# Kernel tuning notes

Hardware: AMD Instinct MI355X
Metric: run time of the kernel (lower is better)

Reference implementation:

```python
import jax, jax.numpy as jnp
import numpy as np

L, N, D, B_, T = 4, 4, 2048, 2, 2048  # num_blocks, expansion_rate, dim, batch, seq


def setup_inputs() -> dict:
    key = jax.random.key(0)
    ks = jax.random.split(key, 12)
    f = lambda k, sh, s=0.02: s * jax.random.normal(k, sh, jnp.float32)
    x = jax.random.normal(ks[0], (B_, T, D), jnp.float32)
    # structural torch inits + small noise so grads/kernels are exercised
    eyecols = jnp.stack([jnp.eye(N, dtype=jnp.float32)[:, [i % N]] for i in range(L)])  # [L,N,1]
    A_m = eyecols + f(ks[1], (L, N, 1), 0.05)
    A_r = jnp.broadcast_to(jnp.eye(N, dtype=jnp.float32), (L, N, N)) + f(ks[2], (L, N, N), 0.05)
    Bp = jnp.ones((L, 1, N), jnp.float32) + f(ks[3], (L, 1, N), 0.05)
    W_m = f(ks[4], (L, D, 1))
    W_r = f(ks[5], (L, D, N))
    W_b = f(ks[6], (L, D, N))
    s_a = 0.01 * jnp.ones((L, 1, 1), jnp.float32)
    s_b = 0.01 * jnp.ones((L, 1, 1), jnp.float32)
    dyn_gamma = jnp.ones((L, D), jnp.float32) + f(ks[7], (L, D), 0.05)   # LayerNorm(bias=False)
    norm_gamma = jnp.ones((L, D), jnp.float32) + f(ks[8], (L, D), 0.05)  # per-block norm weight
    norm_beta = f(ks[9], (L, D))                                          # per-block norm bias
    Wblk = f(ks[10], (L, D, D), 1.0) / np.sqrt(D)                         # block = Linear(D, D)
    bblk = f(ks[11], (L, D))
    return dict(x=x, A_m=A_m, A_r=A_r, Bp=Bp, W_m=W_m, W_r=W_r, W_b=W_b,
                s_a=s_a, s_b=s_b, dyn_gamma=dyn_gamma, norm_gamma=norm_gamma,
                norm_beta=norm_beta, Wblk=Wblk, bblk=bblk)


def _ln(x, gamma, beta=None, eps=1e-5):
    mu = jnp.mean(x, axis=-1, keepdims=True)
    var = jnp.mean(jnp.square(x - mu), axis=-1, keepdims=True)
    y = (x - mu) * jax.lax.rsqrt(var + eps) * gamma
    return y if beta is None else y + beta


def reference(x, A_m, A_r, Bp, W_m, W_r, W_b, s_a, s_b,
              dyn_gamma, norm_gamma, norm_beta, Wblk, bblk):
    # hyper branch (n > 0), dynamic=True, pre_norm=True
    H = jnp.repeat(x[:, :, None, :], N, axis=2)  # [B,T,N,D]
    for i in range(L):
        # ---- width connections ----
        Hn = _ln(H, dyn_gamma[i])                                              # dynamic LN, no bias
        Am = A_m[i] + s_a[i] * jnp.tanh(jnp.einsum('btnd,do->btno', Hn, W_m[i]))  # [B,T,N,1]
        Ar = A_r[i] + s_a[i] * jnp.tanh(jnp.einsum('btnd,dm->btnm', Hn, W_r[i]))  # [B,T,N,N]
        WC = jnp.concatenate([Am, Ar], axis=-1)                                # [B,T,N,1+N]
        Ht = jnp.einsum('btnd,btnm->btdm', H, WC)                              # H^T @ WC
        h = Ht[..., 0]                                                         # [B,T,D]
        H = jnp.swapaxes(Ht[..., 1:], -2, -1)                                  # [B,T,N,D]
        # ---- pre-norm + block ----
        h = _ln(h, norm_gamma[i], norm_beta[i])
        h = jnp.einsum('btd,de->bte', h, Wblk[i]) + bblk[i]
        # ---- depth connections ----
        hn = _ln(h, dyn_gamma[i])
        Bv = Bp[i][0] + s_b[i] * jnp.tanh(jnp.einsum('btd,dn->btn', hn, W_b[i]))  # [B,T,N]
        H = H + h[:, :, None, :] * Bv[..., None]
    return H.sum(axis=2)  # [B,T,D]
```

## Files before the change

### kernel.cpp

```cpp
#include <hip/hip_runtime.h>
#include <hip/hip_bf16.h>


#define DD 2048
#define NN 4
#define LL 4
#define NTOK 4096
#define EPSF 1e-5f
#define STS 80

typedef __attribute__((ext_vector_type(8))) short bf16x8;
typedef __attribute__((ext_vector_type(4))) float f32x4;
typedef __attribute__((ext_vector_type(2))) float f32x2;

__device__ __forceinline__ float bf2f(short u) {
  union { unsigned int i; float f; } v;
  v.i = ((unsigned int)(unsigned short)u) << 16;
  return v.f;
}
__device__ __forceinline__ short f2bf(float f) {
  __hip_bfloat16 h = __float2bfloat16(f);
  short s;
  __builtin_memcpy(&s, &h, 2);
  return s;
}
__device__ __forceinline__ float wred(float v) {
#pragma unroll
  for (int off = 32; off > 0; off >>= 1) v += __shfl_xor(v, off, 64);
  return v;
}
__device__ __forceinline__ void ld16(const void* g, void* l) {
  __builtin_amdgcn_global_load_lds(
      (const __attribute__((address_space(1))) void*)g,
      (__attribute__((address_space(3))) void*)l, 16, 0, 0);
}
__host__ __device__ constexpr int pofs(int k, int l) {
  return k == 0 ? 20 + l * 5
       : k == 1 ? 40 + (l - 1) * 5
       : k == 2 ? 55 + (l - 2) * 5
                : 65;
}

__global__ __launch_bounds__(256) void prep_pack(
    const float* __restrict__ W_m, const float* __restrict__ W_r,
    const float* __restrict__ W_b, const float* __restrict__ dyn_gamma,
    const float* __restrict__ norm_gamma, const float* __restrict__ norm_beta,
    short* __restrict__ gwm, short* __restrict__ gwr, short* __restrict__ gwb,
    float* __restrict__ rb) {
  const int i = blockIdx.x * 256 + threadIdx.x;
  const float g = dyn_gamma[i];
  gwm[i] = f2bf(g * W_m[i]);
  f32x4 r = *(const f32x4*)(W_r + (size_t)i * 4);
  f32x4 b = *(const f32x4*)(W_b + (size_t)i * 4);
  short ro[4], bo[4];
#pragma unroll
  for (int k = 0; k < 4; k++) { ro[k] = f2bf(g * r[k]); bo[k] = f2bf(g * b[k]); }
  *(unsigned long long*)(gwr + (size_t)i * 4) = *(unsigned long long*)ro;
  *(unsigned long long*)(gwb + (size_t)i * 4) = *(unsigned long long*)bo;
  rb[i] = norm_beta[i] / norm_gamma[i];
}

__global__ __launch_bounds__(64) void prep_sums(
    const float* __restrict__ W_m, const float* __restrict__ W_r,
    const float* __restrict__ W_b, const float* __restrict__ dyn_gamma,
    float* __restrict__ S0w, float* __restrict__ T0d) {
  const int l = blockIdx.x;
  const int lane = threadIdx.x;
  float s[5] = {0, 0, 0, 0, 0}, t[4] = {0, 0, 0, 0};
  for (int d = lane; d < DD; d += 64) {
    const float g = dyn_gamma[l * DD + d];
    s[0] += g * W_m[l * DD + d];
    f32x4 r = *(const f32x4*)(W_r + ((size_t)l * DD + d) * 4);
    f32x4 b = *(const f32x4*)(W_b + ((size_t)l * DD + d) * 4);
#pragma unroll
    for (int m = 0; m < 4; m++) { s[1 + m] += g * r[m]; t[m] += g * b[m]; }
  }
#pragma unroll
  for (int m = 0; m < 5; m++) s[m] = wred(s[m]);
#pragma unroll
  for (int n = 0; n < 4; n++) t[n] = wred(t[n]);
  if (lane == 0) {
#pragma unroll
    for (int m = 0; m < 5; m++) S0w[l * 5 + m] = s[m];
#pragma unroll
    for (int n = 0; n < 4; n++) T0d[l * 4 + n] = t[n];
  }
}

__global__ __launch_bounds__(256) void transpose_wblk(
    const float* __restrict__ W, const float* __restrict__ norm_gamma,
    short* __restrict__ Wt) {
  __shared__ float tile[64][65];
  const int blk = blockIdx.z;
  const int c0 = blockIdx.x * 64;
  const int r0 = blockIdx.y * 64;
  const float* Ws = W + (size_t)blk * DD * DD;
  short* Wd = Wt + (size_t)blk * DD * DD;
  const int tx = threadIdx.x & 63, ty = threadIdx.x >> 6;
#pragma unroll
  for (int r = 0; r < 16; r++) {
    const int row = ty + r * 4;
    tile[row][tx] = Ws[(size_t)(r0 + row) * DD + c0 + tx];
  }
  const float gsc = norm_gamma[blk * DD + r0 + tx];
  __syncthreads();
#pragma unroll
  for (int r = 0; r < 16; r++) {
    const int row = ty + r * 4;
    Wd[(size_t)(c0 + row) * DD + r0 + tx] = f2bf(tile[tx][row] * gsc);
  }
}

__global__ __launch_bounds__(256) void row_sums(
    const short* __restrict__ Wt, const float* __restrict__ rb,
    const float* __restrict__ bblk, float* __restrict__ E0,
    float* __restrict__ E1) {
  const int l = blockIdx.y;
  const int e = blockIdx.x * 4 + (threadIdx.x >> 6);
  const int lane = threadIdx.x & 63;
  const short* row = Wt + ((size_t)l * DD + e) * DD;
  const float* rbl = rb + l * DD;
  float s1 = 0.f, s0 = 0.f;
#pragma unroll
  for (int it = 0; it < 4; it++) {
    const int d0 = lane * 8 + it * 512;
    bf16x8 w = *(const bf16x8*)(row + d0);
    f32x4 r0 = *(const f32x4*)(rbl + d0), r1 = *(const f32x4*)(rbl + d0 + 4);
#pragma unroll
    for (int q = 0; q < 8; q++) {
      const float wq = bf2f(w[q]);
      s1 += wq;
      s0 += wq * ((q < 4) ? r0[q] : r1[q - 4]);
    }
  }
  s1 = wred(s1); s0 = wred(s0);
  if (lane == 0) {
    E1[l * DD + e] = s1;
    E0[l * DD + e] = s0 + bblk[l * DD + e];
  }
}

__global__ __launch_bounds__(256) void width0_kernel(
    const float* __restrict__ x, short* __restrict__ b0,
    short* __restrict__ hout, f32x2* __restrict__ tst, float* __restrict__ Cc,
    float* __restrict__ ST, const float* __restrict__ A_m,
    const float* __restrict__ A_r, const short* __restrict__ gwm,
    const short* __restrict__ gwr, const float* __restrict__ s_a,
    const float* __restrict__ S0w) {
  const int wave = threadIdx.x >> 6;
  const int lane = threadIdx.x & 63;
  const int tok = blockIdx.x * 4 + wave;
  const float* xr = x + (size_t)tok * DD;
  short* b0t = b0 + (size_t)tok * DD;

  bf16x8 xb[4];
#pragma unroll
  for (int j = 0; j < 4; j++) {
    const int d0 = lane * 8 + j * 512;
    f32x4 a = *(const f32x4*)(xr + d0);
    f32x4 b = *(const f32x4*)(xr + d0 + 4);
    bf16x8 p;
#pragma unroll
    for (int q = 0; q < 4; q++) { p[q] = f2bf(a[q]); p[4 + q] = f2bf(b[q]); }
    xb[j] = p;
    *(bf16x8*)(b0t + d0) = p;
  }

  float o = 0.f, qq = 0.f, P0[4][5];
#pragma unroll
  for (int l = 0; l < 4; l++)
#pragma unroll
    for (int m = 0; m < 5; m++) P0[l][m] = 0.f;

#pragma unroll
  for (int j = 0; j < 4; j++) {
    const int d0 = lane * 8 + j * 512;
    bf16x8 wmv[4], wrv[4][4];
#pragma unroll
    for (int l = 0; l < 4; l++) {
      wmv[l] = *(const bf16x8*)(gwm + l * DD + d0);
#pragma unroll
      for (int p = 0; p < 4; p++)
        wrv[l][p] = *(const bf16x8*)(gwr + ((size_t)l * DD + d0 + 2 * p) * 4);
    }
#pragma unroll
    for (int q = 0; q < 8; q++) {
      const float hv = bf2f(xb[j][q]);
      o += hv; qq += hv * hv;
#pragma unroll
      for (int l = 0; l < 4; l++) {
        P0[l][0] += hv * bf2f(wmv[l][q]);
#pragma unroll
        for (int m = 0; m < 4; m++)
          P0[l][1 + m] += hv * bf2f(wrv[l][q >> 1][(q & 1) * 4 + m]);
      }
    }
  }
  o = wred(o); qq = wred(qq);
#pragma unroll
  for (int l = 0; l < 4; l++)
#pragma unroll
    for (int m = 0; m < 5; m++) P0[l][m] = wred(P0[l][m]);

  const float sa = s_a[0];
  const float mu = o * (1.f / DD);
  const float inv = rsqrtf(qq * (1.f / DD) - mu * mu + EPSF);
  const float t0 = tanhf(inv * (P0[0][0] - mu * S0w[0]));
  float tm[4];
#pragma unroll
  for (int m = 0; m < 4; m++)
    tm[m] = tanhf(inv * (P0[0][1 + m] - mu * S0w[1 + m]));
  float amSum = 0.f, arCol[4] = {0, 0, 0, 0};
#pragma unroll
  for (int n = 0; n < 4; n++) {
    amSum += A_m[n] + sa * t0;
#pragma unroll
    for (int m = 0; m < 4; m++) arCol[m] += A_r[n * 4 + m] + sa * tm[m];
  }

  if (lane == 0) {
    const float sh = amSum * o;
    const float sh2 = amSum * amSum * qq;
    const float mu2 = sh * (1.f / DD);
    const float inv2 = rsqrtf(sh2 * (1.f / DD) - mu2 * mu2 + EPSF);
    f32x2 t; t[0] = inv2; t[1] = mu2 * inv2;
    tst[tok] = t;
    float* STt = ST + (size_t)tok * STS;
    STt[0] = o;
    STt[4] = qq;
#pragma unroll
    for (int l = 0; l < 4; l++)
#pragma unroll
      for (int m = 0; m < 5; m++) STt[pofs(0, l) + m] = P0[l][m];
    float* Ct = Cc + (size_t)tok * 16;
#pragma unroll
    for (int n = 0; n < 4; n++) Ct[n * 4] = arCol[n];
  }

  short* hw = hout + (size_t)tok * DD;
#pragma unroll
  for (int j = 0; j < 4; j++) {
    const int d0 = lane * 8 + j * 512;
    bf16x8 ho;
#pragma unroll
    for (int q = 0; q < 8; q++) ho[q] = f2bf(amSum * bf2f(xb[j][q]));
    *(bf16x8*)(hw + d0) = ho;
  }
}

__global__ __launch_bounds__(512) void gemm_kernel(
    const short* __restrict__ A, const short* __restrict__ Bt,
    const f32x2* __restrict__ tst, const float* __restrict__ E0,
    const float* __restrict__ E1, short* __restrict__ C) {
  __shared__ short lA[2][128 * 64];
  __shared__ short lB[2][128 * 64];
  const int tid = threadIdx.x;
  const int lane = tid & 63;
  const int wave = tid >> 6;
  const int bid = blockIdx.x;
  const int wg = (bid & 7) * 64 + (bid >> 3);
  const int m0 = (wg & 31) * 128, n0 = (wg >> 5) * 128;
  const int wm = wave >> 2;
  const int wn = wave & 3;

  f32x4 acc[4][2] = {};

#define STAGE(buf, kt)                                                        \
  {                                                                           \
    const int k0 = (kt) * 64;                                                 \
    _Pragma("unroll") for (int c = 0; c < 2; c++) {                           \
      const int idx = c * 512 + tid;                                          \
      const int row = idx >> 3;                                               \
      const int colsw = (((idx & 7) ^ (row & 7)) * 8);                        \
      ld16(A + (size_t)(m0 + row) * DD + k0 + colsw,                          \
           (char*)&lA[buf][0] + idx * 16);                                    \
      ld16(Bt + (size_t)(n0 + row) * DD + k0 + colsw,                         \
           (char*)&lB[buf][0] + idx * 16);                                    \
    }                                                                         \
  }

  STAGE(0, 0);
  __syncthreads();

  for (int kt = 0; kt < 32; ++kt) {
    const int cur = kt & 1;
    if (kt < 31) STAGE(cur ^ 1, kt + 1);
    const char* bufA = (const char*)&lA[cur][0];
    const char* bufB = (const char*)&lB[cur][0];
#pragma unroll
    for (int kk = 0; kk < 2; ++kk) {
      const int gsw = (kk * 64 + (lane >> 4) * 16) ^ ((lane & 7) << 4);
      bf16x8 af[4], bfr[2];
#pragma unroll
      for (int m = 0; m < 4; m++) {
        const int r = wm * 64 + m * 16 + (lane & 15);
        af[m] = *(const bf16x8*)(bufA + r * 128 + gsw);
      }
#pragma unroll
      for (int n = 0; n < 2; n++) {
        const int r = wn * 32 + n * 16 + (lane & 15);
        bfr[n] = *(const bf16x8*)(bufB + r * 128 + gsw);
      }
#pragma unroll
      for (int m = 0; m < 4; m++)
#pragma unroll
        for (int n = 0; n < 2; n++)
          acc[m][n] = __builtin_amdgcn_mfma_f32_16x16x32_bf16(
              af[m], bfr[n], acc[m][n], 0, 0, 0);
    }
    __syncthreads();
  }
#undef STAGE

  float e0c[2], e1c[2];
  int cols[2];
#pragma unroll
  for (int n = 0; n < 2; n++) {
    cols[n] = n0 + wn * 32 + n * 16 + (lane & 15);
    e0c[n] = E0[cols[n]];
    e1c[n] = E1[cols[n]];
  }
#pragma unroll
  for (int m = 0; m < 4; m++) {
    const int rbase = m0 + wm * 64 + m * 16 + ((lane >> 4) << 2);
#pragma unroll
    for (int j = 0; j < 4; j++) {
      const int row = rbase + j;
      const f32x2 iv = tst[row];
#pragma unroll
      for (int n = 0; n < 2; n++)
        C[(size_t)row * DD + cols[n]] =
            f2bf(iv[0] * acc[m][n][j] - iv[1] * e1c[n] + e0c[n]);
    }
  }
}

template <int I>
__global__ __launch_bounds__(256) void fused_dw(
    const short* __restrict__ h2s, const short* __restrict__ b0,
    short* __restrict__ hout, f32x2* __restrict__ tst, float* __restrict__ Cc,
    float* __restrict__ ST, const float* __restrict__ Bp,
    const float* __restrict__ s_b, const float* __restrict__ A_m,
    const float* __restrict__ A_r, const float* __restrict__ s_a,
    const float* __restrict__ S0w, const float* __restrict__ T0d,
    const short* __restrict__ gwm, const short* __restrict__ gwr,
    const short* __restrict__ gwb) {
  constexpr int NB = I + 1;
  constexpr int NP = 3 - I;
  const int wave = threadIdx.x >> 6;
  const int lane = threadIdx.x & 63;
  const int tok = blockIdx.x * 4 + wave;

  const short* vt = h2s + ((size_t)I * NTOK + tok) * DD;
  const short* bases[I + 1];
  bases[0] = b0 + (size_t)tok * DD;
#pragma unroll
  for (int k = 1; k <= I; k++)
    bases[k] = h2s + ((size_t)(k - 1) * NTOK + tok) * DD;

  bf16x8 h2r[4];
#pragma unroll
  for (int j = 0; j < 4; j++)
    h2r[j] = *(const bf16x8*)(vt + lane * 8 + j * 512);

  float o = 0.f;
  float Gr[I + 2] = {};
  float Tb[4] = {0, 0, 0, 0};
  float Pn[NP][5];
#pragma unroll
  for (int li = 0; li < NP; li++)
#pragma unroll
    for (int m = 0; m < 5; m++) Pn[li][m] = 0.f;

#pragma unroll
  for (int j = 0; j < 4; j++) {
    const int d0 = lane * 8 + j * 512;
    bf16x8 bsv[I + 1];
#pragma unroll
    for (int k = 0; k <= I; k++) bsv[k] = *(const bf16x8*)(bases[k] + d0);
    bf16x8 wbv[4];
#pragma unroll
    for (int p = 0; p < 4; p++)
      wbv[p] = *(const bf16x8*)(gwb + ((size_t)I * DD + d0 + 2 * p) * 4);
    bf16x8 wmv[NP], wrv[NP][4];
#pragma unroll
    for (int li = 0; li < NP; li++) {
      const int l = NB + li;
      wmv[li] = *(const bf16x8*)(gwm + l * DD + d0);
#pragma unroll
      for (int p = 0; p < 4; p++)
        wrv[li][p] = *(const bf16x8*)(gwr + ((size_t)l * DD + d0 + 2 * p) * 4);
    }
#pragma unroll
    for (int q = 0; q < 8; q++) {
      const float hv = bf2f(h2r[j][q]);
      o += hv;
      Gr[I + 1] += hv * hv;
#pragma unroll
      for (int k = 0; k <= I; k++) Gr[k] += hv * bf2f(bsv[k][q]);
#pragma unroll
      for (int n = 0; n < 4; n++)
        Tb[n] += hv * bf2f(wbv[q >> 1][(q & 1) * 4 + n]);
#pragma unroll
      for (int li = 0; li < NP; li++) {
        Pn[li][0] += hv * bf2f(wmv[li][q]);
#pragma unroll
        for (int m = 0; m < 4; m++)
          Pn[li][1 + m] += hv * bf2f(wrv[li][q >> 1][(q & 1) * 4 + m]);
      }
    }
  }
  o = wred(o);
#pragma unroll
  for (int k = 0; k <= I + 1; k++) Gr[k] = wred(Gr[k]);
#pragma unroll
  for (int n = 0; n < 4; n++) Tb[n] = wred(Tb[n]);
#pragma unroll
  for (int li = 0; li < NP; li++)
#pragma unroll
    for (int m = 0; m < 5; m++) Pn[li][m] = wred(Pn[li][m]);

  float* STt = ST + (size_t)tok * STS;
  float* Ct = Cc + (size_t)tok * 16;
  float ofull[I + 2], Gf[I + 2][I + 2], Pf[I + 2][5], Cp[4][I + 2];
#pragma unroll
  for (int k = 0; k <= I; k++) ofull[k] = STt[k];
  ofull[I + 1] = o;
#pragma unroll
  for (int k = 0; k <= I; k++)
#pragma unroll
    for (int j2 = 0; j2 <= I; j2++) Gf[k][j2] = STt[4 + k * 4 + j2];
#pragma unroll
  for (int k = 0; k <= I; k++) { Gf[k][I + 1] = Gr[k]; Gf[I + 1][k] = Gr[k]; }
  Gf[I + 1][I + 1] = Gr[I + 1];
#pragma unroll
  for (int k = 0; k <= I; k++)
#pragma unroll
    for (int m = 0; m < 5; m++) Pf[k][m] = STt[pofs(k, NB) + m];
#pragma unroll
  for (int m = 0; m < 5; m++) Pf[I + 1][m] = Pn[0][m];
#pragma unroll
  for (int n = 0; n < 4; n++)
#pragma unroll
    for (int k = 0; k <= I; k++) Cp[n][k] = Ct[n * 4 + k];

  {
    const float mu2 = o * (1.f / DD);
    const float inv2 = rsqrtf(Gr[I + 1] * (1.f / DD) - mu2 * mu2 + EPSF);
    const float sb = s_b[I];
#pragma unroll
    for (int n = 0; n < 4; n++)
      Cp[n][I + 1] = Bp[I * 4 + n] +
                     sb * tanhf(inv2 * (Tb[n] - mu2 * T0d[I * 4 + n]));
  }

  const float sa = s_a[NB];
  float Am[4], Ar[4][4];
#pragma unroll
  for (int n = 0; n < 4; n++) {
    float sH = 0.f, sH2 = 0.f;
#pragma unroll
    for (int k = 0; k <= I + 1; k++) {
      sH += Cp[n][k] * ofull[k];
#pragma unroll
      for (int j2 = 0; j2 <= I + 1; j2++)
        sH2 += Cp[n][k] * Cp[n][j2] * Gf[k][j2];
    }
    const float mu = sH * (1.f / DD);
    const float inv = rsqrtf(sH2 * (1.f / DD) - mu * mu + EPSF);
    float S1[5];
#pragma unroll
    for (int m = 0; m < 5; m++) {
      S1[m] = 0.f;
#pragma unroll
      for (int k = 0; k <= I + 1; k++) S1[m] += Cp[n][k] * Pf[k][m];
    }
    Am[n] = A_m[NB * 4 + n] +
            sa * tanhf(inv * (S1[0] - mu * S0w[NB * 5 + 0]));
#pragma unroll
    for (int m = 0; m < 4; m++)
      Ar[n][m] = A_r[NB * 16 + n * 4 + m] +
                 sa * tanhf(inv * (S1[1 + m] - mu * S0w[NB * 5 + 1 + m]));
  }

  float Cn[4][I + 2], hc[I + 2];
#pragma unroll
  for (int k = 0; k <= I + 1; k++) {
    hc[k] = 0.f;
#pragma unroll
    for (int n = 0; n < 4; n++) hc[k] += Am[n] * Cp[n][k];
  }
#pragma unroll
  for (int mr = 0; mr < 4; mr++)
#pragma unroll
    for (int k = 0; k <= I + 1; k++) {
      float acc = 0.f;
#pragma unroll
      for (int n = 0; n < 4; n++) acc += Ar[n][mr] * Cp[n][k];
      Cn[mr][k] = acc;
    }

  if (lane == 0) {
    float sh = 0.f, sh2 = 0.f;
#pragma unroll
    for (int k = 0; k <= I + 1; k++) {
      sh += hc[k] * ofull[k];
#pragma unroll
      for (int j2 = 0; j2 <= I + 1; j2++) sh2 += hc[k] * hc[j2] * Gf[k][j2];
    }
    const float mu = sh * (1.f / DD);
    const float inv = rsqrtf(sh2 * (1.f / DD) - mu * mu + EPSF);
    f32x2 t; t[0] = inv; t[1] = mu * inv;
    tst[tok] = t;
    STt[I + 1] = o;
#pragma unroll
    for (int k = 0; k <= I + 1; k++) {
      STt[4 + (I + 1) * 4 + k] = Gf[I + 1][k];
      STt[4 + k * 4 + (I + 1)] = Gf[k][I + 1];
    }
#pragma unroll
    for (int li = 1; li < NP; li++)
#pragma unroll
      for (int m = 0; m < 5; m++) STt[pofs(I + 1, NB + li) + m] = Pn[li][m];
#pragma unroll
    for (int n = 0; n < 4; n++)
#pragma unroll
      for (int k = 0; k <= I + 1; k++) Ct[n * 4 + k] = Cn[n][k];
  }

  short* hw = hout + (size_t)tok * DD;
#pragma unroll
  for (int j = 0; j < 4; j++) {
    const int d0 = lane * 8 + j * 512;
    bf16x8 bsv[I + 1];
#pragma unroll
    for (int k = 0; k <= I; k++) bsv[k] = *(const bf16x8*)(bases[k] + d0);
    bf16x8 ho;
#pragma unroll
    for (int q = 0; q < 8; q++) {
      float a = hc[I + 1] * bf2f(h2r[j][q]);
#pragma unroll
      for (int k = 0; k <= I; k++) a += hc[k] * bf2f(bsv[k][q]);
      ho[q] = f2bf(a);
    }
    *(bf16x8*)(hw + d0) = ho;
  }
}

__global__ __launch_bounds__(256) void depth_last(
    const short* __restrict__ h2s, const short* __restrict__ b0,
    float* __restrict__ out, const float* __restrict__ Cc,
    const float* __restrict__ Bp, const float* __restrict__ s_b,
    const float* __restrict__ T0d, const short* __restrict__ gwb) {
  const int wave = threadIdx.x >> 6;
  const int lane = threadIdx.x & 63;
  const int tok = blockIdx.x * 4 + wave;
  const short* vt = h2s + ((size_t)3 * NTOK + tok) * DD;

  bf16x8 h2r[4];
  float s1 = 0.f, s2 = 0.f, Tb[4] = {0, 0, 0, 0};
#pragma unroll
  for (int j = 0; j < 4; j++) {
    const int d0 = lane * 8 + j * 512;
    h2r[j] = *(const bf16x8*)(vt + d0);
    bf16x8 wbv[4];
#pragma unroll
    for (int p = 0; p < 4; p++)
      wbv[p] = *(const bf16x8*)(gwb + ((size_t)3 * DD + d0 + 2 * p) * 4);
#pragma unroll
    for (int q = 0; q < 8; q++) {
      const float hv = bf2f(h2r[j][q]);
      s1 += hv; s2 += hv * hv;
#pragma unroll
      for (int n = 0; n < 4; n++)
        Tb[n] += hv * bf2f(wbv[q >> 1][(q & 1) * 4 + n]);
    }
  }
  s1 = wred(s1); s2 = wred(s2);
#pragma unroll
  for (int n = 0; n < 4; n++) Tb[n] = wred(Tb[n]);

  const float mu = s1 * (1.f / DD);
  const float inv = rsqrtf(s2 * (1.f / DD) - mu * mu + EPSF);
  const float sb = s_b[3];
  float bsum = 0.f;
#pragma unroll
  for (int n = 0; n < 4; n++)
    bsum += Bp[12 + n] + sb * tanhf(inv * (Tb[n] - mu * T0d[12 + n]));

  const float* Ct = Cc + (size_t)tok * 16;
  float e[4];
#pragma unroll
  for (int k = 0; k < 4; k++) {
    e[k] = 0.f;
#pragma unroll
    for (int n = 0; n < 4; n++) e[k] += Ct[n * 4 + k];
  }

  const short* bases[4];
  bases[0] = b0 + (size_t)tok * DD;
#pragma unroll
  for (int k = 1; k < 4; k++)
    bases[k] = h2s + ((size_t)(k - 1) * NTOK + tok) * DD;

  float* orow = out + (size_t)tok * DD;
#pragma unroll
  for (int j = 0; j < 4; j++) {
    const int d0 = lane * 8 + j * 512;
    bf16x8 bsv[4];
#pragma unroll
    for (int k = 0; k < 4; k++) bsv[k] = *(const bf16x8*)(bases[k] + d0);
    f32x4 o0, o1;
#pragma unroll
    for (int q = 0; q < 8; q++) {
      float s = bsum * bf2f(h2r[j][q]);
#pragma unroll
      for (int k = 0; k < 4; k++) s += e[k] * bf2f(bsv[k][q]);
      if (q < 4) o0[q] = s; else o1[q - 4] = s;
    }
    *(f32x4*)(orow + d0) = o0;
    *(f32x4*)(orow + d0 + 4) = o1;
  }
}

extern "C" void kernel_launch(void* const* d_in, const int* in_sizes, int n_in,
                              void* d_out, int out_size, void* d_ws,
                              size_t ws_size, hipStream_t stream) {
  const float* x = (const float*)d_in[0];
  const float* A_m = (const float*)d_in[1];
  const float* A_r = (const float*)d_in[2];
  const float* Bp = (const float*)d_in[3];
  const float* W_m = (const float*)d_in[4];
  const float* W_r = (const float*)d_in[5];
  const float* W_b = (const float*)d_in[6];
  const float* s_a = (const float*)d_in[7];
  const float* s_b = (const float*)d_in[8];
  const float* dyn_gamma = (const float*)d_in[9];
  const float* norm_gamma = (const float*)d_in[10];
  const float* norm_beta = (const float*)d_in[11];
  const float* Wblk = (const float*)d_in[12];
  const float* bblk = (const float*)d_in[13];
  float* out = (float*)d_out;

  char* ws = (char*)d_ws;
  short* b0 = (short*)(ws);
  short* h2s = (short*)(ws + 16777216);
  short* hnorm = (short*)(ws + 83886080);
  char* aux = ws + 100663296;
  short* gwm = (short*)(aux);
  short* gwr = (short*)(aux + 16384);
  short* gwb = (short*)(aux + 81920);
  float* rb = (float*)(aux + 147456);
  float* S0w = (float*)(aux + 180224);
  float* T0d = (float*)(aux + 181248);
  f32x2* tst = (f32x2*)(aux + 182272);
  float* E0 = (float*)(aux + 215040);
  float* E1 = (float*)(aux + 247808);
  float* Cc = (float*)(aux + 280576);
  float* ST = (float*)(aux + 542720);
  short* Wt = (short*)d_out;

  dim3 tb(256);
  prep_pack<<<32, tb, 0, stream>>>(W_m, W_r, W_b, dyn_gamma, norm_gamma,
                                   norm_beta, gwm, gwr, gwb, rb);
  prep_sums<<<4, dim3(64), 0, stream>>>(W_m, W_r, W_b, dyn_gamma, S0w, T0d);
  transpose_wblk<<<dim3(32, 32, 4), tb, 0, stream>>>(Wblk, norm_gamma, Wt);
  row_sums<<<dim3(512, 4), tb, 0, stream>>>(Wt, rb, bblk, E0, E1);
  width0_kernel<<<1024, tb, 0, stream>>>(x, b0, hnorm, tst, Cc, ST, A_m, A_r,
                                         gwm, gwr, s_a, S0w);
  for (int i = 0; i < LL; i++) {
    gemm_kernel<<<512, dim3(512), 0, stream>>>(
        hnorm, Wt + (size_t)i * DD * DD, tst, E0 + i * DD, E1 + i * DD,
        h2s + (size_t)i * NTOK * DD);
    if (i == 0)
      fused_dw<0><<<1024, tb, 0, stream>>>(h2s, b0, hnorm, tst, Cc, ST, Bp,
                                           s_b, A_m, A_r, s_a, S0w, T0d, gwm,
                                           gwr, gwb);
    else if (i == 1)
      fused_dw<1><<<1024, tb, 0, stream>>>(h2s, b0, hnorm, tst, Cc, ST, Bp,
                                           s_b, A_m, A_r, s_a, S0w, T0d, gwm,
                                           gwr, gwb);
    else if (i == 2)
      fused_dw<2><<<1024, tb, 0, stream>>>(h2s, b0, hnorm, tst, Cc, ST, Bp,
                                           s_b, A_m, A_r, s_a, S0w, T0d, gwm,
                                           gwr, gwb);
    else
      depth_last<<<1024, tb, 0, stream>>>(h2s, b0, out, Cc, Bp, s_b, T0d, gwb);
  }
}
```

Before: 326.7 us.

## Use partial vmcnt waits and raw barriers to overlap GEMM staging with MFMA

```diff
diff --git a/kernel.cpp b/kernel.cpp
--- a/kernel.cpp
+++ b/kernel.cpp
@@ -279,38 +279,44 @@
     }                                                                         \
   }
 
+#define COMPUTE(cur)                                                          \
+  {                                                                           \
+    const char* bufA = (const char*)&lA[cur][0];                              \
+    const char* bufB = (const char*)&lB[cur][0];                              \
+    _Pragma("unroll") for (int kk = 0; kk < 2; ++kk) {                        \
+      const int gsw = (kk * 64 + (lane >> 4) * 16) ^ ((lane & 7) << 4);       \
+      bf16x8 af[4], bfr[2];                                                   \
+      _Pragma("unroll") for (int m = 0; m < 4; m++) {                         \
+        const int r = wm * 64 + m * 16 + (lane & 15);                         \
+        af[m] = *(const bf16x8*)(bufA + r * 128 + gsw);                       \
+      }                                                                       \
+      _Pragma("unroll") for (int n = 0; n < 2; n++) {                         \
+        const int r = wn * 32 + n * 16 + (lane & 15);                         \
+        bfr[n] = *(const bf16x8*)(bufB + r * 128 + gsw);                      \
+      }                                                                       \
+      __builtin_amdgcn_s_setprio(1);                                          \
+      _Pragma("unroll") for (int m = 0; m < 4; m++)                           \
+        _Pragma("unroll") for (int n = 0; n < 2; n++)                         \
+          acc[m][n] = __builtin_amdgcn_mfma_f32_16x16x32_bf16(                \
+              af[m], bfr[n], acc[m][n], 0, 0, 0);                             \
+      __builtin_amdgcn_s_setprio(0);                                          \
+    }                                                                         \
+  }
+
   STAGE(0, 0);
-  __syncthreads();
-
-  for (int kt = 0; kt < 32; ++kt) {
+  for (int kt = 0; kt < 31; ++kt) {
     const int cur = kt & 1;
-    if (kt < 31) STAGE(cur ^ 1, kt + 1);
-    const char* bufA = (const char*)&lA[cur][0];
-    const char* bufB = (const char*)&lB[cur][0];
-#pragma unroll
-    for (int kk = 0; kk < 2; ++kk) {
-      const int gsw = (kk * 64 + (lane >> 4) * 16) ^ ((lane & 7) << 4);
-      bf16x8 af[4], bfr[2];
-#pragma unroll
-      for (int m = 0; m < 4; m++) {
-        const int r = wm * 64 + m * 16 + (lane & 15);
-        af[m] = *(const bf16x8*)(bufA + r * 128 + gsw);
-      }
-#pragma unroll
-      for (int n = 0; n < 2; n++) {
-        const int r = wn * 32 + n * 16 + (lane & 15);
-        bfr[n] = *(const bf16x8*)(bufB + r * 128 + gsw);
-      }
-#pragma unroll
-      for (int m = 0; m < 4; m++)
-#pragma unroll
-        for (int n = 0; n < 2; n++)
-          acc[m][n] = __builtin_amdgcn_mfma_f32_16x16x32_bf16(
-              af[m], bfr[n], acc[m][n], 0, 0, 0);
-    }
-    __syncthreads();
-  }
+    STAGE(cur ^ 1, kt + 1);
+    asm volatile("s_waitcnt vmcnt(4)" ::: "memory");
+    asm volatile("s_barrier" ::: "memory");
+    COMPUTE(cur);
+    asm volatile("s_barrier" ::: "memory");
+  }
+  asm volatile("s_waitcnt vmcnt(0)" ::: "memory");
+  asm volatile("s_barrier" ::: "memory");
+  COMPUTE(1);
 #undef STAGE
+#undef COMPUTE
 
   float e0c[2], e1c[2];
   int cols[2];
```

After: 326.6 us, median of 3. Within noise of the previous version (-0.0%).

## Enlarge GEMM tile to 256x128 with triple-buffered interleaved LDS prefetch

Applied to the files above, without the earlier changes.

```diff
diff --git a/kernel.cpp b/kernel.cpp
--- a/kernel.cpp
+++ b/kernel.cpp
@@ -252,65 +252,95 @@
     const short* __restrict__ A, const short* __restrict__ Bt,
     const f32x2* __restrict__ tst, const float* __restrict__ E0,
     const float* __restrict__ E1, short* __restrict__ C) {
-  __shared__ short lA[2][128 * 64];
-  __shared__ short lB[2][128 * 64];
+  __shared__ short lA[3][256 * 64];
+  __shared__ short lB[3][128 * 64];
   const int tid = threadIdx.x;
   const int lane = tid & 63;
   const int wave = tid >> 6;
   const int bid = blockIdx.x;
-  const int wg = (bid & 7) * 64 + (bid >> 3);
-  const int m0 = (wg & 31) * 128, n0 = (wg >> 5) * 128;
+  const int wg = (bid & 7) * 32 + (bid >> 3);
+  const int m0 = (wg & 15) * 256, n0 = (wg >> 4) * 128;
   const int wm = wave >> 2;
   const int wn = wave & 3;
 
-  f32x4 acc[4][2] = {};
-
-#define STAGE(buf, kt)                                                        \
+  f32x4 acc[8][2] = {};
+
+#define STAGEP(buf, kt, p)                                                    \
   {                                                                           \
     const int k0 = (kt) * 64;                                                 \
-    _Pragma("unroll") for (int c = 0; c < 2; c++) {                           \
-      const int idx = c * 512 + tid;                                          \
-      const int row = idx >> 3;                                               \
-      const int colsw = (((idx & 7) ^ (row & 7)) * 8);                        \
-      ld16(A + (size_t)(m0 + row) * DD + k0 + colsw,                          \
-           (char*)&lA[buf][0] + idx * 16);                                    \
-      ld16(Bt + (size_t)(n0 + row) * DD + k0 + colsw,                         \
-           (char*)&lB[buf][0] + idx * 16);                                    \
+    if ((p) < 2) {                                                            \
+      _Pragma("unroll") for (int c = 0; c < 2; c++) {                         \
+        const int idx = ((p) * 2 + c) * 512 + tid;                            \
+        const int row = idx >> 3;                                             \
+        const int colsw = (((idx & 7) ^ (row & 7)) * 8);                      \
+        ld16(A + (size_t)(m0 + row) * DD + k0 + colsw,                        \
+             (char*)&lA[buf][0] + idx * 16);                                  \
+      }                                                                       \
+    } else {                                                                  \
+      _Pragma("unroll") for (int c = 0; c < 2; c++) {                         \
+        const int idx = c * 512 + tid;                                        \
+        const int row = idx >> 3;                                             \
+        const int colsw = (((idx & 7) ^ (row & 7)) * 8);                      \
+        ld16(Bt + (size_t)(n0 + row) * DD + k0 + colsw,                       \
+             (char*)&lB[buf][0] + idx * 16);                                  \
+      }                                                                       \
     }                                                                         \
   }
 
-  STAGE(0, 0);
-  __syncthreads();
-
-  for (int kt = 0; kt < 32; ++kt) {
-    const int cur = kt & 1;
-    if (kt < 31) STAGE(cur ^ 1, kt + 1);
+  STAGEP(0, 0, 0); STAGEP(0, 0, 1); STAGEP(0, 0, 2);
+  STAGEP(1, 1, 0); STAGEP(1, 1, 1); STAGEP(1, 1, 2);
+  asm volatile("s_waitcnt vmcnt(6)" ::: "memory");
+  asm volatile("s_barrier" ::: "memory");
+
+  int cur = 0;
+  for (int t = 0; t < 32; ++t) {
+    int pre = cur + 2; if (pre >= 3) pre -= 3;
     const char* bufA = (const char*)&lA[cur][0];
     const char* bufB = (const char*)&lB[cur][0];
-#pragma unroll
-    for (int kk = 0; kk < 2; ++kk) {
+    bf16x8 bfr[2][2];
+#pragma unroll
+    for (int kk = 0; kk < 2; kk++) {
       const int gsw = (kk * 64 + (lane >> 4) * 16) ^ ((lane & 7) << 4);
-      bf16x8 af[4], bfr[2];
-#pragma unroll
-      for (int m = 0; m < 4; m++) {
-        const int r = wm * 64 + m * 16 + (lane & 15);
-        af[m] = *(const bf16x8*)(bufA + r * 128 + gsw);
-      }
 #pragma unroll
       for (int n = 0; n < 2; n++) {
         const int r = wn * 32 + n * 16 + (lane & 15);
-        bfr[n] = *(const bf16x8*)(bufB + r * 128 + gsw);
+        bfr[n][kk] = *(const bf16x8*)(bufB + r * 128 + gsw);
       }
-#pragma unroll
-      for (int m = 0; m < 4; m++)
+    }
+#pragma unroll
+    for (int q = 0; q < 4; ++q) {
+      bf16x8 af[2][2];
+#pragma unroll
+      for (int kk = 0; kk < 2; kk++) {
+        const int gsw = (kk * 64 + (lane >> 4) * 16) ^ ((lane & 7) << 4);
+#pragma unroll
+        for (int mm = 0; mm < 2; mm++) {
+          const int r = wm * 128 + (2 * q + mm) * 16 + (lane & 15);
+          af[mm][kk] = *(const bf16x8*)(bufA + r * 128 + gsw);
+        }
+      }
+      if (t < 30 && q < 3) STAGEP(pre, t + 2, q);
+      __builtin_amdgcn_s_setprio(1);
+#pragma unroll
+      for (int mm = 0; mm < 2; mm++)
 #pragma unroll
         for (int n = 0; n < 2; n++)
-          acc[m][n] = __builtin_amdgcn_mfma_f32_16x16x32_bf16(
-              af[m], bfr[n], acc[m][n], 0, 0, 0);
-    }
-    __syncthreads();
-  }
-#undef STAGE
+#pragma unroll
+          for (int kk = 0; kk < 2; kk++)
+            acc[2 * q + mm][n] = __builtin_amdgcn_mfma_f32_16x16x32_bf16(
+                af[mm][kk], bfr[n][kk], acc[2 * q + mm][n], 0, 0, 0);
+      __builtin_amdgcn_s_setprio(0);
+    }
+    if (t < 31) {
+      if (t < 30)
+        asm volatile("s_waitcnt vmcnt(6)" ::: "memory");
+      else
+        asm volatile("s_waitcnt vmcnt(0)" ::: "memory");
+      asm volatile("s_barrier" ::: "memory");
+    }
+    cur = cur + 1; if (cur >= 3) cur = 0;
+  }
+#undef STAGEP
 
   float e0c[2], e1c[2];
   int cols[2];
@@ -321,8 +351,8 @@
     e1c[n] = E1[cols[n]];
   }
 #pragma unroll
-  for (int m = 0; m < 4; m++) {
-    const int rbase = m0 + wm * 64 + m * 16 + ((lane >> 4) << 2);
+  for (int m = 0; m < 8; m++) {
+    const int rbase = m0 + wm * 128 + m * 16 + ((lane >> 4) << 2);
 #pragma unroll
     for (int j = 0; j < 4; j++) {
       const int row = rbase + j;
@@ -669,7 +699,7 @@
   width0_kernel<<<1024, tb, 0, stream>>>(x, b0, hnorm, tst, Cc, ST, A_m, A_r,
                                          gwm, gwr, s_a, S0w);
   for (int i = 0; i < LL; i++) {
-    gemm_kernel<<<512, dim3(512), 0, stream>>>(
+    gemm_kernel<<<256, dim3(512), 0, stream>>>(
         hnorm, Wt + (size_t)i * DD * DD, tst, E0 + i * DD, E1 + i * DD,
         h2s + (size_t)i * NTOK * DD);
     if (i == 0)
```

New measurement: 373.1 us. +14.2%, slower.
